# Kernel tuning notes

Measured on AMD Instinct MI355X. Metric: run time of the kernel, lower is better.

Reference implementation:

```python
import jax, jax.numpy as jnp
import numpy as np

K = 6
EPS = 1e-7
BN_EPS = 1e-5


def tagconv(x, row, col, n, lins, bias, mw1, mb1, bng, bnb, mw2, mb2):
    # gcn_norm: symmetric normalization, no self-loops, edge_weight = 1
    deg = jax.ops.segment_sum(jnp.ones(row.shape[0], x.dtype), col, num_segments=n)
    dis = jnp.where(deg > 0, jax.lax.rsqrt(jnp.maximum(deg, 1.0)), 0.0)
    norm = dis[row] * dis[col]  # [E]
    out = x @ lins[0]
    h = x
    for k in range(1, K + 1):
        # message: relu(edge_weight * x_j) + eps, then scatter-add to destination
        msg = jax.nn.relu(norm[:, None] * h[row]) + EPS  # [E, C]
        h = jax.ops.segment_sum(msg, col, num_segments=n)
        out = out + h @ lins[k]
    out = out + bias
    # MLP: Linear -> BatchNorm1d(eval: running mean 0, var 1) -> ReLU -> Dropout(eval) -> Linear
    z = out @ mw1 + mb1
    z = bng * (z * (1.0 / np.sqrt(1.0 + BN_EPS))) + bnb
    z = jax.nn.relu(z)
    return z @ mw2 + mb2


def setup_inputs() -> dict:
    key = jax.random.key(0)
    ks = jax.random.split(key, 8)
    N, E, F, H, C = 50000, 800000, 128, 128, 64
    s = 0.05
    return {
        "x": jax.random.normal(ks[0], (N, F), jnp.float32),
        "edge_index": jax.random.randint(ks[1], (2, E), 0, N, jnp.int64),
        "lins1": jax.random.normal(ks[2], (K + 1, F, H), jnp.float32) * s,
        "bias1": jnp.zeros((H,), jnp.float32),
        "m1w1": jax.random.normal(ks[3], (H, 2 * H), jnp.float32) * s,
        "m1b1": jnp.zeros((2 * H,), jnp.float32),
        "bn1g": jnp.ones((2 * H,), jnp.float32),
        "bn1b": jnp.zeros((2 * H,), jnp.float32),
        "m1w2": jax.random.normal(ks[4], (2 * H, H), jnp.float32) * s,
        "m1b2": jnp.zeros((H,), jnp.float32),
        "lins2": jax.random.normal(ks[5], (K + 1, H, C), jnp.float32) * s,
        "bias2": jnp.zeros((C,), jnp.float32),
        "m2w1": jax.random.normal(ks[6], (C, 2 * C), jnp.float32) * s,
        "m2b1": jnp.zeros((2 * C,), jnp.float32),
        "bn2g": jnp.ones((2 * C,), jnp.float32),
        "bn2b": jnp.zeros((2 * C,), jnp.float32),
        "m2w2": jax.random.normal(ks[7], (2 * C, C), jnp.float32) * s,
        "m2b2": jnp.zeros((C,), jnp.float32),
    }


def reference(x, edge_index, lins1, bias1, m1w1, m1b1, bn1g, bn1b, m1w2, m1b2,
              lins2, bias2, m2w1, m2b1, bn2g, bn2b, m2w2, m2b2):
    n = x.shape[0]
    row, col = edge_index[0], edge_index[1]
    h = tagconv(x, row, col, n, lins1, bias1, m1w1, m1b1, bn1g, bn1b, m1w2, m1b2)
    h = jax.nn.relu(h)  # dropout is identity in eval mode
    return tagconv(h, row, col, n, lins2, bias2, m2w1, m2b1, bn2g, bn2b, m2w2, m2b2)
```

## Files before the change

### kernel.cpp

```cpp
#include <hip/hip_runtime.h>
#include <hip/hip_bf16.h>


#define EPS_MSG 1e-7f
#define BNSCALE 0.9999950000374997f
#define LO_INV 0.0009765625f

typedef _Float16 half_t;
typedef _Float16 f16x8 __attribute__((ext_vector_type(8)));
typedef float f32x4 __attribute__((ext_vector_type(4)));

__device__ __forceinline__ void gld16(const char* g, char* l) {
    __builtin_amdgcn_global_load_lds(
        (const __attribute__((address_space(1))) void*)g,
        (__attribute__((address_space(3))) void*)l, 16, 0, 0);
}

__device__ __forceinline__ float hlo(unsigned p) {
    unsigned short u = (unsigned short)(p & 0xffffu);
    half_t h;
    __builtin_memcpy(&h, &u, 2);
    return (float)h;
}
__device__ __forceinline__ float hhi(unsigned p) {
    unsigned short u = (unsigned short)(p >> 16);
    half_t h;
    __builtin_memcpy(&h, &u, 2);
    return (float)h;
}
__device__ __forceinline__ unsigned fpack2(float x, float y) {
    half_t a = (half_t)x, b = (half_t)y;
    unsigned short ua, ub;
    __builtin_memcpy(&ua, &a, 2);
    __builtin_memcpy(&ub, &b, 2);
    return (unsigned)ua | ((unsigned)ub << 16);
}


__global__ void zero_i32(int* __restrict__ p, int n) {
    int i = blockIdx.x * blockDim.x + threadIdx.x;
    if (i < n) p[i] = 0;
}

__global__ void count_deg(const int* __restrict__ col, int* __restrict__ deg, int E) {
    int e = blockIdx.x * blockDim.x + threadIdx.x;
    if (e < E) atomicAdd(&deg[col[e]], 1);
}

__global__ void compute_dis_s(const int* __restrict__ deg, float* __restrict__ dis,
                              float* __restrict__ s, float* __restrict__ rs, int N) {
    int v = blockIdx.x * blockDim.x + threadIdx.x;
    if (v >= N) return;
    int d = deg[v];
    float di = (d > 0) ? rsqrtf((float)d) : 0.f;
    dis[v] = di;
    s[v] = (d > 0) ? di : 1.f;
    rs[v] = (d > 0) ? sqrtf((float)d) : 1.f;
}

__global__ void scan_blk(const int* __restrict__ deg, int* __restrict__ off,
                         int* __restrict__ bsum, int N) {
    __shared__ int sm[1024];
    int i = blockIdx.x * 1024 + threadIdx.x;
    sm[threadIdx.x] = (i < N) ? deg[i] : 0;
    __syncthreads();
    for (int ofs = 1; ofs < 1024; ofs <<= 1) {
        int t = (threadIdx.x >= (unsigned)ofs) ? sm[threadIdx.x - ofs] : 0;
        __syncthreads();
        sm[threadIdx.x] += t;
        __syncthreads();
    }
    if (i < N) off[i + 1] = sm[threadIdx.x];
    if (threadIdx.x == 0) bsum[blockIdx.x] = sm[1023];
}

__global__ void scan_top(int* __restrict__ bsum, int nb) {
    if (threadIdx.x == 0 && blockIdx.x == 0) {
        int a = 0;
        for (int b = 0; b < nb; ++b) {
            int t = bsum[b];
            bsum[b] = a;
            a += t;
        }
    }
}

__global__ void scan_add(int* __restrict__ off, const int* __restrict__ bsum, int N) {
    int i = blockIdx.x * 1024 + threadIdx.x;
    if (i < N) off[i + 1] += bsum[blockIdx.x];
    if (i == 0) off[0] = 0;
}

__global__ void fill_edges(const int* __restrict__ row, const int* __restrict__ col,
                           const int* __restrict__ off, int* __restrict__ cur,
                           unsigned short* __restrict__ esrc, int E) {
    int e = blockIdx.x * blockDim.x + threadIdx.x;
    if (e >= E) return;
    int c = col[e];
    int pos = off[c] + atomicAdd(&cur[c], 1);
    esrc[pos] = (unsigned short)row[e];
}


__global__ void conv_xg(const float* __restrict__ x, half_t* __restrict__ slab,
                        half_t* __restrict__ g0, const float* __restrict__ dis,
                        const float* __restrict__ s, int total) {
    int i = blockIdx.x * blockDim.x + threadIdx.x;
    if (i >= total) return;
    int v = i >> 7, c = i & 127;
    float xv = x[i];
    slab[(size_t)v * 896 + c] = (half_t)(s[v] * xv);
    g0[i] = (half_t)(dis[v] * fmaxf(xv, 0.f));
}

__device__ __forceinline__ void wcv(const float* __restrict__ in, half_t* __restrict__ oh,
                                    half_t* __restrict__ ol, int nm, int K, int Nn, int i) {
    int KT = nm * K;
    int n = i / KT;
    int rem = i - n * KT;
    int km = rem / K, k = rem - km * K;
    float w = in[(size_t)km * K * Nn + (size_t)k * Nn + n];
    half_t h = (half_t)w;
    oh[i] = h;
    ol[i] = (half_t)((w - (float)h) * 1024.f);
}

__global__ void conv_all(const float* l1, const float* l2, const float* a1, const float* b1,
                         const float* a2, const float* b2, half_t* W1h, half_t* W1l,
                         half_t* W2h, half_t* W2l, half_t* M1ah, half_t* M1al, half_t* M1bh,
                         half_t* M1bl, half_t* M2ah, half_t* M2al, half_t* M2bh,
                         half_t* M2bl) {
    int i = blockIdx.x * blockDim.x + threadIdx.x;
    if (i < 114688) {
        wcv(l1, W1h, W1l, 7, 128, 128, i);
    } else if (i < 172032) {
        int j = i - 114688;
        int np = j >> 7, k = j & 127;
        int km = np >> 6, n = np & 63;
        float w = l2[(size_t)km * 128 * 64 + (size_t)k * 64 + n];
        half_t h = (half_t)w;
        W2h[j] = h;
        W2l[j] = (half_t)((w - (float)h) * 1024.f);
    } else if (i < 204800) {
        wcv(a1, M1ah, M1al, 1, 128, 256, i - 172032);
    } else if (i < 237568) {
        wcv(b1, M1bh, M1bl, 1, 256, 128, i - 204800);
    } else if (i < 245760) {
        wcv(a2, M2ah, M2al, 1, 64, 128, i - 237568);
    } else if (i < 253952) {
        wcv(b2, M2bh, M2bl, 1, 128, 64, i - 245760);
    }
}

__global__ void conv_trows(const float* __restrict__ l2, float* __restrict__ T) {
    int j = threadIdx.x >> 6;
    int c = threadIdx.x & 63;
    if (j >= 6) return;
    float a = 0.f;
    for (int k = j + 1; k <= 6; ++k)
        for (int kk = 0; kk < 128; ++kk) a += l2[(size_t)k * 128 * 64 + kk * 64 + c];
    T[j * 64 + c] = a;
}


__global__ void __launch_bounds__(256) prop(const unsigned* __restrict__ gin, int idl,
                                            unsigned* __restrict__ gout, int odl,
                                            const float* __restrict__ dis,
                                            const int* __restrict__ off,
                                            const unsigned short* __restrict__ esrc, int N) {
    const int lane = threadIdx.x & 63;
    const int w = threadIdx.x >> 6;
    const int stride = gridDim.x * 4;
    for (int v = blockIdx.x * 4 + w; v < N; v += stride) {
        int s = off[v], e = off[v + 1];
        float2 A0 = {0.f, 0.f}, A1 = {0.f, 0.f}, A2 = {0.f, 0.f}, A3 = {0.f, 0.f};
        float2 A4 = {0.f, 0.f}, A5 = {0.f, 0.f}, A6 = {0.f, 0.f}, A7 = {0.f, 0.f};
        for (int i = s; i < e; i += 8) {
            unsigned p[8];
            int ok[8];
#pragma unroll
            for (int j = 0; j < 8; ++j) {
                int ij = i + j;
                ok[j] = ij < e;
                int idx = ok[j] ? ij : e - 1;
                p[j] = gin[esrc[idx] * idl + lane];
            }
            A0.x += ok[0] ? hlo(p[0]) : 0.f; A0.y += ok[0] ? hhi(p[0]) : 0.f;
            A1.x += ok[1] ? hlo(p[1]) : 0.f; A1.y += ok[1] ? hhi(p[1]) : 0.f;
            A2.x += ok[2] ? hlo(p[2]) : 0.f; A2.y += ok[2] ? hhi(p[2]) : 0.f;
            A3.x += ok[3] ? hlo(p[3]) : 0.f; A3.y += ok[3] ? hhi(p[3]) : 0.f;
            A4.x += ok[4] ? hlo(p[4]) : 0.f; A4.y += ok[4] ? hhi(p[4]) : 0.f;
            A5.x += ok[5] ? hlo(p[5]) : 0.f; A5.y += ok[5] ? hhi(p[5]) : 0.f;
            A6.x += ok[6] ? hlo(p[6]) : 0.f; A6.y += ok[6] ? hhi(p[6]) : 0.f;
            A7.x += ok[7] ? hlo(p[7]) : 0.f; A7.y += ok[7] ? hhi(p[7]) : 0.f;
        }
        float ax = ((A0.x + A1.x) + (A2.x + A3.x)) + ((A4.x + A5.x) + (A6.x + A7.x));
        float ay = ((A0.y + A1.y) + (A2.y + A3.y)) + ((A4.y + A5.y) + (A6.y + A7.y));
        float dv = dis[v];
        float ce = (float)(e - s) * EPS_MSG;
        float hx = fmaf(dv, ax, ce);
        float hy = fmaf(dv, ay, ce);
        gout[v * odl + lane] = fpack2(dv * hx, dv * hy);
    }
}


template <int FINAL>
__global__ void __launch_bounds__(256) prop64(
    const half_t* __restrict__ uin, int ldu, const half_t* __restrict__ pj, int ldp,
    half_t* __restrict__ uout, int ldo, const float* __restrict__ dis,
    const int* __restrict__ off, const unsigned short* __restrict__ esrc,
    const float* __restrict__ tj, const float* __restrict__ bias2, int N) {
    const int c = threadIdx.x & 63;
    const int w = threadIdx.x >> 6;
    const int stride = gridDim.x * 4;
    for (int v = blockIdx.x * 4 + w; v < N; v += stride) {
        int s = off[v], e = off[v + 1];
        float a0 = 0.f, a1 = 0.f, a2 = 0.f, a3 = 0.f;
        float a4 = 0.f, a5 = 0.f, a6 = 0.f, a7 = 0.f;
        for (int i = s; i < e; i += 8) {
            float q[8];
            int ok[8];
#pragma unroll
            for (int j = 0; j < 8; ++j) {
                int ij = i + j;
                ok[j] = ij < e;
                int idx = ok[j] ? ij : e - 1;
                q[j] = (float)uin[(size_t)esrc[idx] * ldu + c];
            }
            a0 += ok[0] ? q[0] : 0.f;
            a1 += ok[1] ? q[1] : 0.f;
            a2 += ok[2] ? q[2] : 0.f;
            a3 += ok[3] ? q[3] : 0.f;
            a4 += ok[4] ? q[4] : 0.f;
            a5 += ok[5] ? q[5] : 0.f;
            a6 += ok[6] ? q[6] : 0.f;
            a7 += ok[7] ? q[7] : 0.f;
        }
        float acc = ((a0 + a1) + (a2 + a3)) + ((a4 + a5) + (a6 + a7));
        float dv = dis[v];
        float base = (float)pj[(size_t)v * ldp + c] + (float)(e - s) * EPS_MSG * tj[c];
        float u = fmaf(dv, acc, base);
        if (FINAL)
            uout[(size_t)v * ldo + c] = (half_t)(u + bias2[c]);
        else
            uout[(size_t)v * ldo + c] = (half_t)(dv * u);
    }
}


template <int BN, int OUTF32>
__global__ __launch_bounds__(256) void gemm(
    int M, int kiters, const half_t* __restrict__ A, int lda,
    const half_t* __restrict__ Bhp, const half_t* __restrict__ Blp, int ldb, int noff,
    void* __restrict__ Cp, int ldc, const float* __restrict__ rs, int epi,
    const float* __restrict__ bias, const float* __restrict__ bng,
    const float* __restrict__ bnb) {
    constexpr int BM = 64, BK = 64;
    constexpr int WC = (BN == 128) ? 2 : 1;
    constexpr int WROWS = BM / (4 / WC);
    constexpr int MF = WROWS / 16;
    constexpr int NF = 4;
    constexpr int ABY = BM * BK * 2;
    constexpr int BBY = BN * BK * 2;
    constexpr int BUFBY = ABY + 2 * BBY;
    constexpr int ACW = (ABY / 1024) / 4;
    constexpr int BCW = (BBY / 1024) / 4;

    __shared__ char lds[2][BUFBY];

    const int tid = threadIdx.x;
    const int lane = tid & 63;
    const int w = tid >> 6;
    const int wr = w / WC, wc = w % WC;
    const int m0 = blockIdx.x * BM;
    const int n0 = blockIdx.y * BN + noff;
    const int l15 = lane & 15, lq = lane >> 4;
    const int lr8 = lane >> 3, lc8 = lane & 7;

    const char* gA = (const char*)A;
    const char* gBh = (const char*)Bhp;
    const char* gBl = (const char*)Blp;
    const size_t ldaB = (size_t)lda * 2, ldbB = (size_t)ldb * 2;

    auto stage = [&](int kt, int buf) {
        const int k0b = kt * BK * 2;
        char* base = lds[0] + buf * BUFBY;
#pragma unroll
        for (int i = 0; i < ACW; ++i) {
            int c = w * ACW + i;
            int r = c * 8 + lr8;
            int gv = m0 + r;
            if (gv >= M) gv = M - 1;
            int sc = (lc8 ^ (r & 7)) << 4;
            gld16(gA + (size_t)gv * ldaB + k0b + sc, base + c * 1024);
        }
#pragma unroll
        for (int i = 0; i < BCW; ++i) {
            int c = w * BCW + i;
            int r = c * 8 + lr8;
            int sc = (lc8 ^ (r & 7)) << 4;
            size_t goff = (size_t)(n0 + r) * ldbB + k0b + sc;
            gld16(gBh + goff, base + ABY + c * 1024);
            gld16(gBl + goff, base + ABY + BBY + c * 1024);
        }
    };

    f32x4 acch[MF][NF], accl[MF][NF];
#pragma unroll
    for (int fm = 0; fm < MF; ++fm)
#pragma unroll
        for (int fn = 0; fn < NF; ++fn) {
            acch[fm][fn] = (f32x4){0.f, 0.f, 0.f, 0.f};
            accl[fm][fn] = (f32x4){0.f, 0.f, 0.f, 0.f};
        }

    auto compute = [&](int buf) {
        const char* Ab = lds[0] + buf * BUFBY;
        const char* Bhb = Ab + ABY;
        const char* Blb = Ab + ABY + BBY;
#pragma unroll
        for (int ks = 0; ks < 2; ++ks) {
            const int cc = ks * 4 + lq;
            f16x8 af[MF];
#pragma unroll
            for (int fm = 0; fm < MF; ++fm) {
                int r = wr * WROWS + fm * 16 + l15;
                af[fm] = *(const f16x8*)(Ab + r * 128 + ((cc ^ (r & 7)) << 4));
            }
#pragma unroll
            for (int fn = 0; fn < NF; ++fn) {
                int r = wc * 64 + fn * 16 + l15;
                int o = r * 128 + ((cc ^ (r & 7)) << 4);
                f16x8 bhv = *(const f16x8*)(Bhb + o);
                f16x8 blv = *(const f16x8*)(Blb + o);
#pragma unroll
                for (int fm = 0; fm < MF; ++fm) {
                    acch[fm][fn] =
                        __builtin_amdgcn_mfma_f32_16x16x32_f16(af[fm], bhv, acch[fm][fn], 0, 0, 0);
                    accl[fm][fn] =
                        __builtin_amdgcn_mfma_f32_16x16x32_f16(af[fm], blv, accl[fm][fn], 0, 0, 0);
                }
            }
        }
    };

    stage(0, 0);
    int buf = 0;
    for (int kt = 0; kt < kiters; ++kt) {
        __syncthreads();
        if (kt + 1 < kiters) stage(kt + 1, buf ^ 1);
        compute(buf);
        buf ^= 1;
    }

#pragma unroll
    for (int fm = 0; fm < MF; ++fm)
#pragma unroll
        for (int fn = 0; fn < NF; ++fn)
#pragma unroll
            for (int i = 0; i < 4; ++i) {
                int gr = m0 + wr * WROWS + fm * 16 + (lane >> 4) * 4 + i;
                if (gr >= M) continue;
                int gc = n0 + wc * 64 + fn * 16 + (lane & 15);
                float v = acch[fm][fn][i] + accl[fm][fn][i] * LO_INV;
                if (rs) v *= rs[gr];
                if (epi == 1) {
                    v += bias[gc];
                } else if (epi == 2) {
                    v = bng[gc] * ((v + bias[gc]) * BNSCALE) + bnb[gc];
                    v = fmaxf(v, 0.f);
                } else if (epi == 3) {
                    v = fmaxf(v + bias[gc], 0.f);
                }
                if (OUTF32)
                    ((float*)Cp)[(size_t)gr * ldc + gc] = v;
                else
                    ((half_t*)Cp)[(size_t)gr * ldc + gc] = (half_t)v;
            }
}

extern "C" void kernel_launch(void* const* d_in, const int* in_sizes, int n_in,
                              void* d_out, int out_size, void* d_ws, size_t ws_size,
                              hipStream_t stream) {
    const float* x     = (const float*)d_in[0];
    const int*   ei    = (const int*)d_in[1];
    const float* lins1 = (const float*)d_in[2];
    const float* bias1 = (const float*)d_in[3];
    const float* m1w1  = (const float*)d_in[4];
    const float* m1b1  = (const float*)d_in[5];
    const float* bn1g  = (const float*)d_in[6];
    const float* bn1b  = (const float*)d_in[7];
    const float* m1w2  = (const float*)d_in[8];
    const float* m1b2  = (const float*)d_in[9];
    const float* lins2 = (const float*)d_in[10];
    const float* bias2 = (const float*)d_in[11];
    const float* m2w1  = (const float*)d_in[12];
    const float* m2b1  = (const float*)d_in[13];
    const float* bn2g  = (const float*)d_in[14];
    const float* bn2b  = (const float*)d_in[15];
    const float* m2w2  = (const float*)d_in[16];
    const float* m2b2  = (const float*)d_in[17];
    float* out = (float*)d_out;

    const int N = in_sizes[0] / 128;
    const int E = in_sizes[1] / 2;
    const int* row = ei;
    const int* col = ei + E;

    char* ws = (char*)d_ws;
    size_t o = 0;
    auto alloc = [&](size_t bytes) {
        void* p = ws + o;
        o += (bytes + 255) & ~(size_t)255;
        return p;
    };
    int*            deg  = (int*)alloc((size_t)N * 4);
    int*            cur  = (int*)alloc((size_t)N * 4);
    float*          dis  = (float*)alloc((size_t)N * 4);
    float*          sA   = (float*)alloc((size_t)N * 4);
    float*          rsA  = (float*)alloc((size_t)N * 4);
    int*            off  = (int*)alloc((size_t)(N + 1) * 4);
    int*            bsum = (int*)alloc(1024 * 4);
    float*          Trow = (float*)alloc(6 * 64 * 4);
    unsigned short* esrc = (unsigned short*)alloc((size_t)E * 2);
    half_t* g0    = (half_t*)alloc((size_t)N * 128 * 2);
    half_t* ACC   = (half_t*)alloc((size_t)N * 128 * 2);
    half_t* Z     = (half_t*)alloc((size_t)N * 256 * 2);
    half_t* H1    = (half_t*)alloc((size_t)N * 128 * 2);
    half_t* ACC2  = (half_t*)alloc((size_t)N * 64 * 2);
    half_t* Wc1h  = (half_t*)alloc((size_t)128 * 896 * 2);
    half_t* Wc1l  = (half_t*)alloc((size_t)128 * 896 * 2);
    half_t* Wc2h  = (half_t*)alloc((size_t)448 * 128 * 2);
    half_t* Wc2l  = (half_t*)alloc((size_t)448 * 128 * 2);
    half_t* Wm1ah = (half_t*)alloc((size_t)256 * 128 * 2);
    half_t* Wm1al = (half_t*)alloc((size_t)256 * 128 * 2);
    half_t* Wm1bh = (half_t*)alloc((size_t)128 * 256 * 2);
    half_t* Wm1bl = (half_t*)alloc((size_t)128 * 256 * 2);
    half_t* Wm2ah = (half_t*)alloc((size_t)128 * 64 * 2);
    half_t* Wm2al = (half_t*)alloc((size_t)128 * 64 * 2);
    half_t* Wm2bh = (half_t*)alloc((size_t)64 * 128 * 2);
    half_t* Wm2bl = (half_t*)alloc((size_t)64 * 128 * 2);
    half_t* slab  = (half_t*)alloc((size_t)N * 896 * 2);
    (void)ws_size;

    const int TPB = 256;
    const int nb = (N + 1023) / 1024;
    zero_i32<<<(N + TPB - 1) / TPB, TPB, 0, stream>>>(deg, N);
    zero_i32<<<(N + TPB - 1) / TPB, TPB, 0, stream>>>(cur, N);
    count_deg<<<(E + TPB - 1) / TPB, TPB, 0, stream>>>(col, deg, E);
    compute_dis_s<<<(N + TPB - 1) / TPB, TPB, 0, stream>>>(deg, dis, sA, rsA, N);
    scan_blk<<<nb, 1024, 0, stream>>>(deg, off, bsum, N);
    scan_top<<<1, 64, 0, stream>>>(bsum, nb);
    scan_add<<<nb, 1024, 0, stream>>>(off, bsum, N);
    fill_edges<<<(E + TPB - 1) / TPB, TPB, 0, stream>>>(row, col, off, cur, esrc, E);
    conv_all<<<(253952 + TPB - 1) / TPB, TPB, 0, stream>>>(
        lins1, lins2, m1w1, m1w2, m2w1, m2w2, Wc1h, Wc1l, Wc2h, Wc2l, Wm1ah, Wm1al, Wm1bh,
        Wm1bl, Wm2ah, Wm2al, Wm2bh, Wm2bl);
    conv_trows<<<1, 384, 0, stream>>>(lins2, Trow);
    conv_xg<<<(N * 128 + TPB - 1) / TPB, TPB, 0, stream>>>(x, slab, g0, dis, sA, N * 128);

    unsigned* slabU = (unsigned*)slab;
    unsigned* g0U = (unsigned*)g0;
    const int HG = (N + 63) / 64;

    prop<<<2048, 256, 0, stream>>>(g0U, 64, slabU + 64, 448, dis, off, esrc, N);
    for (int k = 2; k <= 6; ++k)
        prop<<<2048, 256, 0, stream>>>(slabU + (size_t)(k - 1) * 64, 448,
                                       slabU + (size_t)k * 64, 448, dis, off, esrc, N);
    gemm<128, 0><<<dim3(HG, 1), 256, 0, stream>>>(
        N, 14, slab, 896, Wc1h, Wc1l, 896, 0, ACC, 128, rsA, 1, bias1, nullptr, nullptr);
    gemm<128, 0><<<dim3(HG, 2), 256, 0, stream>>>(
        N, 2, ACC, 128, Wm1ah, Wm1al, 128, 0, Z, 256, nullptr, 2, m1b1, bn1g, bn1b);
    gemm<128, 0><<<dim3(HG, 1), 256, 0, stream>>>(
        N, 4, Z, 256, Wm1bh, Wm1bl, 256, 0, H1, 128, nullptr, 3, m1b2, nullptr, nullptr);

    gemm<64, 0><<<dim3(HG, 6), 256, 0, stream>>>(
        N, 2, H1, 128, Wc2h, Wc2l, 128, 0, slab, 448, nullptr, 0, nullptr, nullptr, nullptr);
    gemm<64, 0><<<dim3(HG, 1), 256, 0, stream>>>(
        N, 2, H1, 128, Wc2h, Wc2l, 128, 384, slab, 448, dis, 0, nullptr, nullptr, nullptr);

    half_t* ub0 = g0;
    half_t* ub1 = g0 + (size_t)N * 64;
    prop64<0><<<2048, 256, 0, stream>>>(slab + 384, 448, slab + 320, 448, ub0, 64, dis, off,
                                        esrc, Trow + 5 * 64, nullptr, N);
    prop64<0><<<2048, 256, 0, stream>>>(ub0, 64, slab + 256, 448, ub1, 64, dis, off, esrc,
                                        Trow + 4 * 64, nullptr, N);
    prop64<0><<<2048, 256, 0, stream>>>(ub1, 64, slab + 192, 448, ub0, 64, dis, off, esrc,
                                        Trow + 3 * 64, nullptr, N);
    prop64<0><<<2048, 256, 0, stream>>>(ub0, 64, slab + 128, 448, ub1, 64, dis, off, esrc,
                                        Trow + 2 * 64, nullptr, N);
    prop64<0><<<2048, 256, 0, stream>>>(ub1, 64, slab + 64, 448, ub0, 64, dis, off, esrc,
                                        Trow + 1 * 64, nullptr, N);
    prop64<1><<<2048, 256, 0, stream>>>(ub0, 64, slab, 448, ACC2, 64, dis, off, esrc,
                                        Trow + 0 * 64, bias2, N);

    gemm<128, 0><<<dim3(HG, 1), 256, 0, stream>>>(
        N, 1, ACC2, 64, Wm2ah, Wm2al, 64, 0, Z, 128, nullptr, 2, m2b1, bn2g, bn2b);
    gemm<64, 1><<<dim3(HG, 1), 256, 0, stream>>>(
        N, 2, Z, 128, Wm2bh, Wm2bl, 128, 0, out, 64, nullptr, 1, m2b2, nullptr, nullptr);
}
```

Baseline: 713.0 us.

## Bucket edges by destination group and source block for locality-aware propagation

```diff
diff --git a/kernel.cpp b/kernel.cpp
--- a/kernel.cpp
+++ b/kernel.cpp
@@ -45,6 +45,14 @@
 __global__ void count_deg(const int* __restrict__ col, int* __restrict__ deg, int E) {
     int e = blockIdx.x * blockDim.x + threadIdx.x;
     if (e < E) atomicAdd(&deg[col[e]], 1);
+}
+
+__global__ void ehist(const int* __restrict__ row, const int* __restrict__ col,
+                      int* __restrict__ hist, int E) {
+    int e = blockIdx.x * blockDim.x + threadIdx.x;
+    if (e >= E) return;
+    int key = (col[e] >> 4) * 16 + (row[e] >> 12);
+    atomicAdd(&hist[key], 1);
 }
 
 __global__ void compute_dis_s(const int* __restrict__ deg, float* __restrict__ dis,
@@ -58,11 +66,11 @@
     rs[v] = (d > 0) ? sqrtf((float)d) : 1.f;
 }
 
-__global__ void scan_blk(const int* __restrict__ deg, int* __restrict__ off,
+__global__ void scan_blk(const int* __restrict__ in, int* __restrict__ off,
                          int* __restrict__ bsum, int N) {
     __shared__ int sm[1024];
     int i = blockIdx.x * 1024 + threadIdx.x;
-    sm[threadIdx.x] = (i < N) ? deg[i] : 0;
+    sm[threadIdx.x] = (i < N) ? in[i] : 0;
     __syncthreads();
     for (int ofs = 1; ofs < 1024; ofs <<= 1) {
         int t = (threadIdx.x >= (unsigned)ofs) ? sm[threadIdx.x - ofs] : 0;
@@ -91,14 +99,15 @@
     if (i == 0) off[0] = 0;
 }
 
-__global__ void fill_edges(const int* __restrict__ row, const int* __restrict__ col,
-                           const int* __restrict__ off, int* __restrict__ cur,
-                           unsigned short* __restrict__ esrc, int E) {
+__global__ void fill_erec(const int* __restrict__ row, const int* __restrict__ col,
+                          const int* __restrict__ cellOff, int* __restrict__ cur,
+                          unsigned* __restrict__ erec, int E) {
     int e = blockIdx.x * blockDim.x + threadIdx.x;
     if (e >= E) return;
-    int c = col[e];
-    int pos = off[c] + atomicAdd(&cur[c], 1);
-    esrc[pos] = (unsigned short)row[e];
+    int r = row[e], c = col[e];
+    int key = (c >> 4) * 16 + (r >> 12);
+    int pos = cellOff[key] + atomicAdd(&cur[key], 1);
+    erec[pos] = (unsigned)r | ((unsigned)(c & 15) << 16);
 }
 
 
@@ -153,98 +162,112 @@
 }
 
 __global__ void conv_trows(const float* __restrict__ l2, float* __restrict__ T) {
-    int j = threadIdx.x >> 6;
+    __shared__ float sm[256];
+    int j = blockIdx.x;
     int c = threadIdx.x & 63;
-    if (j >= 6) return;
+    int part = threadIdx.x >> 6;
     float a = 0.f;
     for (int k = j + 1; k <= 6; ++k)
-        for (int kk = 0; kk < 128; ++kk) a += l2[(size_t)k * 128 * 64 + kk * 64 + c];
-    T[j * 64 + c] = a;
-}
-
-
-__global__ void __launch_bounds__(256) prop(const unsigned* __restrict__ gin, int idl,
-                                            unsigned* __restrict__ gout, int odl,
-                                            const float* __restrict__ dis,
-                                            const int* __restrict__ off,
-                                            const unsigned short* __restrict__ esrc, int N) {
-    const int lane = threadIdx.x & 63;
-    const int w = threadIdx.x >> 6;
-    const int stride = gridDim.x * 4;
-    for (int v = blockIdx.x * 4 + w; v < N; v += stride) {
-        int s = off[v], e = off[v + 1];
-        float2 A0 = {0.f, 0.f}, A1 = {0.f, 0.f}, A2 = {0.f, 0.f}, A3 = {0.f, 0.f};
-        float2 A4 = {0.f, 0.f}, A5 = {0.f, 0.f}, A6 = {0.f, 0.f}, A7 = {0.f, 0.f};
-        for (int i = s; i < e; i += 8) {
-            unsigned p[8];
-            int ok[8];
-#pragma unroll
-            for (int j = 0; j < 8; ++j) {
-                int ij = i + j;
-                ok[j] = ij < e;
-                int idx = ok[j] ? ij : e - 1;
-                p[j] = gin[esrc[idx] * idl + lane];
+        for (int kk = part; kk < 128; kk += 4)
+            a += l2[(size_t)k * 128 * 64 + kk * 64 + c];
+    sm[threadIdx.x] = a;
+    __syncthreads();
+    if (part == 0) T[j * 64 + c] = (sm[c] + sm[64 + c]) + (sm[128 + c] + sm[192 + c]);
+}
+
+
+__global__ void __launch_bounds__(512) bprop128(
+    const unsigned* __restrict__ gin, int idl, unsigned* __restrict__ gout, int odl,
+    const float* __restrict__ dis, const int* __restrict__ deg,
+    const unsigned* __restrict__ erec, const int* __restrict__ cellOff, int ngroups,
+    int N) {
+    __shared__ float acc[8][16][128];
+    const int w = threadIdx.x >> 6, lane = threadIdx.x & 63;
+    const int g = blockIdx.x * 8 + w;
+    if (g >= ngroups) return;
+    float* a = &acc[w][0][0];
+#pragma unroll
+    for (int d = 0; d < 16; ++d) {
+        a[d * 128 + lane] = 0.f;
+        a[d * 128 + 64 + lane] = 0.f;
+    }
+    const int s = cellOff[g * 16], e = cellOff[(g + 1) * 16];
+    for (int i = s; i < e; i += 8) {
+        unsigned rr[8], pp[8];
+        int ok[8];
+#pragma unroll
+        for (int j = 0; j < 8; ++j) {
+            int ij = i + j;
+            ok[j] = ij < e;
+            rr[j] = erec[ok[j] ? ij : e - 1];
+            pp[j] = gin[(rr[j] & 0xffffu) * idl + lane];
+        }
+#pragma unroll
+        for (int j = 0; j < 8; ++j) {
+            if (ok[j]) {
+                float* ad = a + (rr[j] >> 16) * 128;
+                ad[lane] += hlo(pp[j]);
+                ad[64 + lane] += hhi(pp[j]);
             }
-            A0.x += ok[0] ? hlo(p[0]) : 0.f; A0.y += ok[0] ? hhi(p[0]) : 0.f;
-            A1.x += ok[1] ? hlo(p[1]) : 0.f; A1.y += ok[1] ? hhi(p[1]) : 0.f;
-            A2.x += ok[2] ? hlo(p[2]) : 0.f; A2.y += ok[2] ? hhi(p[2]) : 0.f;
-            A3.x += ok[3] ? hlo(p[3]) : 0.f; A3.y += ok[3] ? hhi(p[3]) : 0.f;
-            A4.x += ok[4] ? hlo(p[4]) : 0.f; A4.y += ok[4] ? hhi(p[4]) : 0.f;
-            A5.x += ok[5] ? hlo(p[5]) : 0.f; A5.y += ok[5] ? hhi(p[5]) : 0.f;
-            A6.x += ok[6] ? hlo(p[6]) : 0.f; A6.y += ok[6] ? hhi(p[6]) : 0.f;
-            A7.x += ok[7] ? hlo(p[7]) : 0.f; A7.y += ok[7] ? hhi(p[7]) : 0.f;
-        }
-        float ax = ((A0.x + A1.x) + (A2.x + A3.x)) + ((A4.x + A5.x) + (A6.x + A7.x));
-        float ay = ((A0.y + A1.y) + (A2.y + A3.y)) + ((A4.y + A5.y) + (A6.y + A7.y));
+        }
+    }
+    const int v0 = g * 16;
+#pragma unroll
+    for (int d = 0; d < 16; ++d) {
+        int v = v0 + d;
+        if (v >= N) break;
         float dv = dis[v];
-        float ce = (float)(e - s) * EPS_MSG;
-        float hx = fmaf(dv, ax, ce);
-        float hy = fmaf(dv, ay, ce);
-        gout[v * odl + lane] = fpack2(dv * hx, dv * hy);
+        float ce = (float)deg[v] * EPS_MSG;
+        float hx = fmaf(dv, a[d * 128 + lane], ce);
+        float hy = fmaf(dv, a[d * 128 + 64 + lane], ce);
+        gout[(size_t)v * odl + lane] = fpack2(dv * hx, dv * hy);
     }
 }
 
 
 template <int FINAL>
-__global__ void __launch_bounds__(256) prop64(
-    const half_t* __restrict__ uin, int ldu, const half_t* __restrict__ pj, int ldp,
+__global__ void __launch_bounds__(512) bprop64(
+    const half_t* __restrict__ uin, int ldu, const half_t* __restrict__ pj,
     half_t* __restrict__ uout, int ldo, const float* __restrict__ dis,
-    const int* __restrict__ off, const unsigned short* __restrict__ esrc,
-    const float* __restrict__ tj, const float* __restrict__ bias2, int N) {
-    const int c = threadIdx.x & 63;
-    const int w = threadIdx.x >> 6;
-    const int stride = gridDim.x * 4;
-    for (int v = blockIdx.x * 4 + w; v < N; v += stride) {
-        int s = off[v], e = off[v + 1];
-        float a0 = 0.f, a1 = 0.f, a2 = 0.f, a3 = 0.f;
-        float a4 = 0.f, a5 = 0.f, a6 = 0.f, a7 = 0.f;
-        for (int i = s; i < e; i += 8) {
-            float q[8];
-            int ok[8];
-#pragma unroll
-            for (int j = 0; j < 8; ++j) {
-                int ij = i + j;
-                ok[j] = ij < e;
-                int idx = ok[j] ? ij : e - 1;
-                q[j] = (float)uin[(size_t)esrc[idx] * ldu + c];
-            }
-            a0 += ok[0] ? q[0] : 0.f;
-            a1 += ok[1] ? q[1] : 0.f;
-            a2 += ok[2] ? q[2] : 0.f;
-            a3 += ok[3] ? q[3] : 0.f;
-            a4 += ok[4] ? q[4] : 0.f;
-            a5 += ok[5] ? q[5] : 0.f;
-            a6 += ok[6] ? q[6] : 0.f;
-            a7 += ok[7] ? q[7] : 0.f;
-        }
-        float acc = ((a0 + a1) + (a2 + a3)) + ((a4 + a5) + (a6 + a7));
+    const int* __restrict__ deg, const unsigned* __restrict__ erec,
+    const int* __restrict__ cellOff, const float* __restrict__ tj,
+    const float* __restrict__ bias2, int ngroups, int N) {
+    __shared__ float acc[8][16][64];
+    const int w = threadIdx.x >> 6, lane = threadIdx.x & 63;
+    const int g = blockIdx.x * 8 + w;
+    if (g >= ngroups) return;
+    float* a = &acc[w][0][0];
+#pragma unroll
+    for (int d = 0; d < 16; ++d) a[d * 64 + lane] = 0.f;
+    const int s = cellOff[g * 16], e = cellOff[(g + 1) * 16];
+    for (int i = s; i < e; i += 8) {
+        unsigned rr[8];
+        float qq[8];
+        int ok[8];
+#pragma unroll
+        for (int j = 0; j < 8; ++j) {
+            int ij = i + j;
+            ok[j] = ij < e;
+            rr[j] = erec[ok[j] ? ij : e - 1];
+            qq[j] = (float)uin[(size_t)(rr[j] & 0xffffu) * ldu + lane];
+        }
+#pragma unroll
+        for (int j = 0; j < 8; ++j) {
+            if (ok[j]) a[(rr[j] >> 16) * 64 + lane] += qq[j];
+        }
+    }
+    const int v0 = g * 16;
+#pragma unroll
+    for (int d = 0; d < 16; ++d) {
+        int v = v0 + d;
+        if (v >= N) break;
         float dv = dis[v];
-        float base = (float)pj[(size_t)v * ldp + c] + (float)(e - s) * EPS_MSG * tj[c];
-        float u = fmaf(dv, acc, base);
+        float base = (float)pj[(size_t)v * 448 + lane] + (float)deg[v] * EPS_MSG * tj[lane];
+        float u = fmaf(dv, a[d * 64 + lane], base);
         if (FINAL)
-            uout[(size_t)v * ldo + c] = (half_t)(u + bias2[c]);
+            uout[(size_t)v * ldo + lane] = (half_t)(u + bias2[lane]);
         else
-            uout[(size_t)v * ldo + c] = (half_t)(dv * u);
+            uout[(size_t)v * ldo + lane] = (half_t)(dv * u);
     }
 }
 
@@ -407,6 +430,8 @@
     const int E = in_sizes[1] / 2;
     const int* row = ei;
     const int* col = ei + E;
+    const int ngroups = (N + 15) / 16;
+    const int ncells = ngroups * 16;
 
     char* ws = (char*)d_ws;
     size_t o = 0;
@@ -415,15 +440,16 @@
         o += (bytes + 255) & ~(size_t)255;
         return p;
     };
-    int*            deg  = (int*)alloc((size_t)N * 4);
-    int*            cur  = (int*)alloc((size_t)N * 4);
-    float*          dis  = (float*)alloc((size_t)N * 4);
-    float*          sA   = (float*)alloc((size_t)N * 4);
-    float*          rsA  = (float*)alloc((size_t)N * 4);
-    int*            off  = (int*)alloc((size_t)(N + 1) * 4);
-    int*            bsum = (int*)alloc(1024 * 4);
-    float*          Trow = (float*)alloc(6 * 64 * 4);
-    unsigned short* esrc = (unsigned short*)alloc((size_t)E * 2);
+    int*      deg  = (int*)alloc((size_t)N * 4);
+    int*      hist = (int*)alloc((size_t)ncells * 4);
+    int*      cur  = (int*)alloc((size_t)ncells * 4);
+    float*    dis  = (float*)alloc((size_t)N * 4);
+    float*    sA   = (float*)alloc((size_t)N * 4);
+    float*    rsA  = (float*)alloc((size_t)N * 4);
+    int*      coff = (int*)alloc((size_t)(ncells + 1) * 4);
+    int*      bsum = (int*)alloc(1024 * 4);
+    float*    Trow = (float*)alloc(6 * 64 * 4);
+    unsigned* erec = (unsigned*)alloc((size_t)E * 4);
     half_t* g0    = (half_t*)alloc((size_t)N * 128 * 2);
     half_t* ACC   = (half_t*)alloc((size_t)N * 128 * 2);
     half_t* Z     = (half_t*)alloc((size_t)N * 256 * 2);
@@ -445,29 +471,33 @@
     (void)ws_size;
 
     const int TPB = 256;
-    const int nb = (N + 1023) / 1024;
+    const int nbc = (ncells + 1023) / 1024;
     zero_i32<<<(N + TPB - 1) / TPB, TPB, 0, stream>>>(deg, N);
-    zero_i32<<<(N + TPB - 1) / TPB, TPB, 0, stream>>>(cur, N);
+    zero_i32<<<(ncells + TPB - 1) / TPB, TPB, 0, stream>>>(hist, ncells);
+    zero_i32<<<(ncells + TPB - 1) / TPB, TPB, 0, stream>>>(cur, ncells);
     count_deg<<<(E + TPB - 1) / TPB, TPB, 0, stream>>>(col, deg, E);
+    ehist<<<(E + TPB - 1) / TPB, TPB, 0, stream>>>(row, col, hist, E);
     compute_dis_s<<<(N + TPB - 1) / TPB, TPB, 0, stream>>>(deg, dis, sA, rsA, N);
-    scan_blk<<<nb, 1024, 0, stream>>>(deg, off, bsum, N);
-    scan_top<<<1, 64, 0, stream>>>(bsum, nb);
-    scan_add<<<nb, 1024, 0, stream>>>(off, bsum, N);
-    fill_edges<<<(E + TPB - 1) / TPB, TPB, 0, stream>>>(row, col, off, cur, esrc, E);
+    scan_blk<<<nbc, 1024, 0, stream>>>(hist, coff, bsum, ncells);
+    scan_top<<<1, 64, 0, stream>>>(bsum, nbc);
+    scan_add<<<nbc, 1024, 0, stream>>>(coff, bsum, ncells);
+    fill_erec<<<(E + TPB - 1) / TPB, TPB, 0, stream>>>(row, col, coff, cur, erec, E);
     conv_all<<<(253952 + TPB - 1) / TPB, TPB, 0, stream>>>(
         lins1, lins2, m1w1, m1w2, m2w1, m2w2, Wc1h, Wc1l, Wc2h, Wc2l, Wm1ah, Wm1al, Wm1bh,
         Wm1bl, Wm2ah, Wm2al, Wm2bh, Wm2bl);
-    conv_trows<<<1, 384, 0, stream>>>(lins2, Trow);
+    conv_trows<<<6, 256, 0, stream>>>(lins2, Trow);
     conv_xg<<<(N * 128 + TPB - 1) / TPB, TPB, 0, stream>>>(x, slab, g0, dis, sA, N * 128);
 
     unsigned* slabU = (unsigned*)slab;
     unsigned* g0U = (unsigned*)g0;
     const int HG = (N + 63) / 64;
-
-    prop<<<2048, 256, 0, stream>>>(g0U, 64, slabU + 64, 448, dis, off, esrc, N);
+    const int PB = (ngroups + 7) / 8;
+
+    bprop128<<<PB, 512, 0, stream>>>(g0U, 64, slabU + 64, 448, dis, deg, erec, coff, ngroups, N);
     for (int k = 2; k <= 6; ++k)
-        prop<<<2048, 256, 0, stream>>>(slabU + (size_t)(k - 1) * 64, 448,
-                                       slabU + (size_t)k * 64, 448, dis, off, esrc, N);
+        bprop128<<<PB, 512, 0, stream>>>(slabU + (size_t)(k - 1) * 64, 448,
+                                         slabU + (size_t)k * 64, 448, dis, deg, erec, coff,
+                                         ngroups, N);
     gemm<128, 0><<<dim3(HG, 1), 256, 0, stream>>>(
         N, 14, slab, 896, Wc1h, Wc1l, 896, 0, ACC, 128, rsA, 1, bias1, nullptr, nullptr);
     gemm<128, 0><<<dim3(HG, 2), 256, 0, stream>>>(
@@ -482,18 +512,18 @@
 
     half_t* ub0 = g0;
     half_t* ub1 = g0 + (size_t)N * 64;
-    prop64<0><<<2048, 256, 0, stream>>>(slab + 384, 448, slab + 320, 448, ub0, 64, dis, off,
-                                        esrc, Trow + 5 * 64, nullptr, N);
-    prop64<0><<<2048, 256, 0, stream>>>(ub0, 64, slab + 256, 448, ub1, 64, dis, off, esrc,
-                                        Trow + 4 * 64, nullptr, N);
-    prop64<0><<<2048, 256, 0, stream>>>(ub1, 64, slab + 192, 448, ub0, 64, dis, off, esrc,
-                                        Trow + 3 * 64, nullptr, N);
-    prop64<0><<<2048, 256, 0, stream>>>(ub0, 64, slab + 128, 448, ub1, 64, dis, off, esrc,
-                                        Trow + 2 * 64, nullptr, N);
-    prop64<0><<<2048, 256, 0, stream>>>(ub1, 64, slab + 64, 448, ub0, 64, dis, off, esrc,
-                                        Trow + 1 * 64, nullptr, N);
-    prop64<1><<<2048, 256, 0, stream>>>(ub0, 64, slab, 448, ACC2, 64, dis, off, esrc,
-                                        Trow + 0 * 64, bias2, N);
+    bprop64<0><<<PB, 512, 0, stream>>>(slab + 384, 448, slab + 320, ub0, 64, dis, deg, erec,
+                                       coff, Trow + 5 * 64, nullptr, ngroups, N);
+    bprop64<0><<<PB, 512, 0, stream>>>(ub0, 64, slab + 256, ub1, 64, dis, deg, erec, coff,
+                                       Trow + 4 * 64, nullptr, ngroups, N);
+    bprop64<0><<<PB, 512, 0, stream>>>(ub1, 64, slab + 192, ub0, 64, dis, deg, erec, coff,
+                                       Trow + 3 * 64, nullptr, ngroups, N);
+    bprop64<0><<<PB, 512, 0, stream>>>(ub0, 64, slab + 128, ub1, 64, dis, deg, erec, coff,
+                                       Trow + 2 * 64, nullptr, ngroups, N);
+    bprop64<0><<<PB, 512, 0, stream>>>(ub1, 64, slab + 64, ub0, 64, dis, deg, erec, coff,
+                                       Trow + 1 * 64, nullptr, ngroups, N);
+    bprop64<1><<<PB, 512, 0, stream>>>(ub0, 64, slab, ACC2, 64, dis, deg, erec, coff,
+                                       Trow + 0 * 64, bias2, ngroups, N);
 
     gemm<128, 0><<<dim3(HG, 1), 256, 0, stream>>>(
         N, 1, ACC2, 64, Wm2ah, Wm2al, 64, 0, Z, 128, nullptr, 2, m2b1, bn2g, bn2b);
```

Result: slower. 1.162 ms (+63.0%).
